# Optimization experiments

Hardware: AMD Instinct MI355X
Metric: run time of the kernel (lower is better)

The kernel has to match this reference:

```python
import jax, jax.numpy as jnp
import numpy as np

N_SRC, N_TGT, N_EDGES = 100000, 50000, 600000
IN_CH, OUT_CH = 128, 128
NUM_EDGE_TYPES, NUM_NODE_TYPES = 7, 4


def setup_inputs() -> dict:
    key = jax.random.key(0)
    ks = jax.random.split(key, 9)
    x_src = jax.random.normal(ks[0], (N_SRC, IN_CH), dtype=jnp.float32)
    x_target = jax.random.normal(ks[1], (N_TGT, IN_CH), dtype=jnp.float32)
    # PyG Linear: y = x @ W.T (+ b); W has shape (out, in)
    rel_w = jax.random.normal(ks[2], (NUM_EDGE_TYPES, OUT_CH, IN_CH), dtype=jnp.float32) * 0.05
    root_w = jax.random.normal(ks[3], (NUM_NODE_TYPES, OUT_CH, IN_CH), dtype=jnp.float32) * 0.05
    root_b = jax.random.normal(ks[4], (NUM_NODE_TYPES, OUT_CH), dtype=jnp.float32) * 0.05
    edge_src = jax.random.randint(ks[5], (N_EDGES,), 0, N_SRC, dtype=jnp.int32)
    edge_dst = jax.random.randint(ks[6], (N_EDGES,), 0, N_TGT, dtype=jnp.int32)
    edge_type = jax.random.randint(ks[7], (N_EDGES,), 0, NUM_EDGE_TYPES, dtype=jnp.int32)
    target_node_type = jax.random.randint(ks[8], (N_TGT,), 0, NUM_NODE_TYPES, dtype=jnp.int32)
    return {
        "x_src": x_src, "x_target": x_target,
        "rel_w": rel_w, "root_w": root_w, "root_b": root_b,
        "edge_src": edge_src, "edge_dst": edge_dst,
        "edge_type": edge_type, "target_node_type": target_node_type,
    }


def reference(x_src, x_target, rel_w, root_w, root_b,
              edge_src, edge_dst, edge_type, target_node_type):
    n_tgt = x_target.shape[0]
    num_rel = rel_w.shape[0]
    num_ntypes = root_w.shape[0]
    # Gather source features once for all edges: (E, in)
    msg = x_src[edge_src]
    out = jnp.zeros((n_tgt, rel_w.shape[1]), dtype=x_target.dtype)
    # Per-relation linear transform + scatter-MEAN over that relation's edges
    # (matches one propagate(aggr='mean') call per edge type: nodes with no
    #  incoming edges of type r contribute 0 for that relation).
    for r in range(num_rel):
        mask = (edge_type == r).astype(msg.dtype)  # (E,)
        y = (msg * mask[:, None]) @ rel_w[r].T     # (E, out)
        s = jax.ops.segment_sum(y, edge_dst, num_segments=n_tgt)
        cnt = jax.ops.segment_sum(mask, edge_dst, num_segments=n_tgt)
        out = out + s / jnp.maximum(cnt, 1.0)[:, None]
    # Per-node-type root linear (with bias), masked add
    for t in range(num_ntypes):
        m = (target_node_type == t)
        root = x_target @ root_w[t].T + root_b[t]
        out = out + jnp.where(m[:, None], root, 0.0)
    return out
```

## Files before the change

### kernel.cpp

```cpp
#include <hip/hip_runtime.h>

#define NSRC 100000
#define NTGT 50000
#define NE   600000
#define CH   128
#define NREL 7
#define NTYP 4
#define NP   (NREL * NTGT)
#define NB   ((NP + 1023) / 1024)
#define MAXBLK ((NTGT + 63) / 64)

typedef __attribute__((ext_vector_type(4))) float f32x4;
typedef __attribute__((ext_vector_type(8))) short bf16x8;
typedef unsigned int uint;
typedef unsigned short ushort;

static constexpr size_t A256(size_t x) { return (x + 255) & ~(size_t)255; }
static constexpr size_t CNT_O   = 0;
static constexpr size_t TCNT_O  = A256(CNT_O + (size_t)NP * 4);
static constexpr size_t ZERO_END= TCNT_O + 256;
static constexpr size_t BSE_O   = ZERO_END;
static constexpr size_t BSR_O   = A256(BSE_O + (size_t)NB * 4);
static constexpr size_t BBE_O   = A256(BSR_O + (size_t)NB * 4);
static constexpr size_t BBR_O   = A256(BBE_O + (size_t)NB * 4);
static constexpr size_t CUR_O   = A256(BBR_O + (size_t)NB * 4);
static constexpr size_t PLO_O   = A256(CUR_O + (size_t)NP * 4);
static constexpr size_t PN_O    = A256(PLO_O + (size_t)NP * 4);
static constexpr size_t PINV_O  = A256(PN_O + (size_t)NP * 4);
static constexpr size_t PDST_O  = A256(PINV_O + (size_t)NP * 4);
static constexpr size_t RELO_O  = A256(PDST_O + (size_t)NP * 4);
static constexpr size_t BKT_O   = A256(RELO_O + 64);
static constexpr size_t SEDGE_O = A256(BKT_O + (size_t)NTYP * NTGT * 4);
static constexpr size_t WB_O    = A256(SEDGE_O + (size_t)NE * 4);
static constexpr size_t XB_O    = A256(WB_O + (size_t)(NREL + NTYP) * CH * CH * 2);
static constexpr size_t XTB_O   = A256(XB_O + (size_t)NSRC * CH * 2);

__device__ __forceinline__ uint bfpack(float a, float b) {
  uint ua = __float_as_uint(a); ua = (ua + 0x7fff + ((ua >> 16) & 1)) >> 16;
  uint ub = __float_as_uint(b); ub = (ub + 0x7fff + ((ub >> 16) & 1)) >> 16;
  return ua | (ub << 16);
}
__device__ __forceinline__ ushort f2b(float x) {
  uint u = __float_as_uint(x);
  return (ushort)((u + 0x7fff + ((u >> 16) & 1)) >> 16);
}
__device__ __forceinline__ float bl(uint u) { return __uint_as_float(u << 16); }
__device__ __forceinline__ float bh(uint u) { return __uint_as_float(u & 0xffff0000u); }

__global__ void k_count(const int* __restrict__ edst, const int* __restrict__ etyp,
                        int* __restrict__ cnt) {
  int i = blockIdx.x * 256 + threadIdx.x;
  if (i < NE) atomicAdd(&cnt[etyp[i] * NTGT + edst[i]], 1);
}

__global__ void k_bucket(const int* __restrict__ ntyp, int* __restrict__ tcnt,
                         int* __restrict__ bucket) {
  __shared__ int lcnt[NTYP];
  __shared__ int lbase[NTYP];
  int v = blockIdx.x * 256 + threadIdx.x;
  if (threadIdx.x < NTYP) lcnt[threadIdx.x] = 0;
  __syncthreads();
  int t = 0, r = 0;
  bool ok = v < NTGT;
  if (ok) { t = ntyp[v]; r = atomicAdd(&lcnt[t], 1); }
  __syncthreads();
  if (threadIdx.x < NTYP) lbase[threadIdx.x] = atomicAdd(&tcnt[threadIdx.x], lcnt[threadIdx.x]);
  __syncthreads();
  if (ok) bucket[t * NTGT + lbase[t] + r] = v;
}

__global__ __launch_bounds__(256) void k_s1(const int* __restrict__ cnt,
                                            int* __restrict__ bsE, int* __restrict__ bsR) {
  __shared__ int sE[256], sR[256];
  int t = threadIdx.x, p0 = blockIdx.x * 1024 + t * 4;
  int e = 0, r = 0;
#pragma unroll
  for (int j = 0; j < 4; ++j) {
    int p = p0 + j;
    if (p < NP) { int c = cnt[p]; e += c; r += (c > 0); }
  }
  sE[t] = e; sR[t] = r; __syncthreads();
  for (int s = 128; s > 0; s >>= 1) {
    if (t < s) { sE[t] += sE[t + s]; sR[t] += sR[t + s]; }
    __syncthreads();
  }
  if (t == 0) { bsE[blockIdx.x] = sE[0]; bsR[blockIdx.x] = sR[0]; }
}

__global__ __launch_bounds__(512) void k_s2(const int* __restrict__ bsE, const int* __restrict__ bsR,
                                            int* __restrict__ bbE, int* __restrict__ bbR,
                                            int* __restrict__ reloff) {
  __shared__ int sE[512], sR[512];
  int t = threadIdx.x;
  int e = (t < NB) ? bsE[t] : 0;
  int r = (t < NB) ? bsR[t] : 0;
  sE[t] = e; sR[t] = r; __syncthreads();
  for (int s = 1; s < 512; s <<= 1) {
    int ae = 0, ar = 0;
    if (t >= s) { ae = sE[t - s]; ar = sR[t - s]; }
    __syncthreads();
    sE[t] += ae; sR[t] += ar;
    __syncthreads();
  }
  if (t < NB) { bbE[t] = sE[t] - e; bbR[t] = sR[t] - r; }
  if (t == NB - 1) reloff[NREL] = sR[t];
}

__global__ __launch_bounds__(256) void k_s3(const int* __restrict__ cnt,
    const int* __restrict__ bbE, const int* __restrict__ bbR,
    int* __restrict__ cur, int* __restrict__ plo, int* __restrict__ pn,
    float* __restrict__ pinv, int* __restrict__ pdst, int* __restrict__ reloff) {
  __shared__ int sE[256], sR[256];
  int t = threadIdx.x, p0 = blockIdx.x * 1024 + t * 4;
  int c[4]; int e = 0, r = 0;
#pragma unroll
  for (int j = 0; j < 4; ++j) {
    int p = p0 + j;
    c[j] = (p < NP) ? cnt[p] : 0;
    e += c[j]; r += (c[j] > 0);
  }
  sE[t] = e; sR[t] = r; __syncthreads();
  for (int s = 1; s < 256; s <<= 1) {
    int ae = 0, ar = 0;
    if (t >= s) { ae = sE[t - s]; ar = sR[t - s]; }
    __syncthreads();
    sE[t] += ae; sR[t] += ar;
    __syncthreads();
  }
  int baseE = bbE[blockIdx.x] + sE[t] - e;
  int baseR = bbR[blockIdx.x] + sR[t] - r;
#pragma unroll
  for (int j = 0; j < 4; ++j) {
    int p = p0 + j;
    if (p < NP) {
      cur[p] = baseE;
      if ((p % NTGT) == 0) reloff[p / NTGT] = baseR;
      if (c[j] > 0) {
        plo[baseR] = baseE; pn[baseR] = c[j];
        pinv[baseR] = 1.0f / (float)c[j];
        pdst[baseR] = p % NTGT;
        baseR++;
      }
      baseE += c[j];
    }
  }
}

__global__ void k_esort(const int* __restrict__ esrc, const int* __restrict__ edst,
                        const int* __restrict__ etyp, int* __restrict__ cur,
                        int* __restrict__ sedge) {
  int i = blockIdx.x * 256 + threadIdx.x;
  if (i < NE) {
    int p = etyp[i] * NTGT + edst[i];
    int pos = atomicAdd(&cur[p], 1);
    sedge[pos] = esrc[i];
  }
}

__global__ void k_conv(const float* __restrict__ xsrc, const float* __restrict__ xt,
                       const float* __restrict__ relw, const float* __restrict__ rootw,
                       ushort* __restrict__ xb, ushort* __restrict__ xtb,
                       ushort* __restrict__ wb) {
  const long long NXB = (long long)NSRC * CH / 4;
  const long long NXT = (long long)NTGT * CH / 4;
  const long long NWR = (long long)NREL * CH * CH / 4;
  const long long NWT = (long long)NTYP * CH * CH / 4;
  long long i4 = (long long)blockIdx.x * 256 + threadIdx.x;
  const float* src; ushort* dst; long long off;
  if (i4 < NXB) { src = xsrc; dst = xb; off = i4; }
  else if (i4 < NXB + NXT) { src = xt; dst = xtb; off = i4 - NXB; }
  else if (i4 < NXB + NXT + NWR) { src = relw; dst = wb; off = i4 - NXB - NXT; }
  else if (i4 < NXB + NXT + NWR + NWT) {
    src = rootw; dst = wb + (size_t)NREL * CH * CH; off = i4 - NXB - NXT - NWR;
  } else return;
  float4 v = *(const float4*)(src + off * 4);
  uint lo = (uint)f2b(v.x) | ((uint)f2b(v.y) << 16);
  uint hi = (uint)f2b(v.z) | ((uint)f2b(v.w) << 16);
  uint2 o = make_uint2(lo, hi);
  *(uint2*)(dst + off * 4) = o;
}

__global__ void k_init(const float* __restrict__ rootb, const int* __restrict__ ntyp,
                       float* __restrict__ out) {
  int idx = blockIdx.x * 256 + threadIdx.x;
  if (idx >= NTGT * 32) return;
  int v = idx >> 5, c4 = (idx & 31) << 2;
  int t = ntyp[v];
  *(float4*)(out + (size_t)v * CH + c4) = *(const float4*)(rootb + (size_t)t * CH + c4);
}

__device__ __forceinline__ void mfma_tail(const ushort* strip, const ushort* W,
                                          int m, int quad, const int* rowmap,
                                          float* __restrict__ out) {
  bf16x8 aF[4];
#pragma unroll
  for (int ks = 0; ks < 4; ++ks) {
    int c = ks * 4 + quad;
    aF[ks] = *(const bf16x8*)&strip[(m * 16 + (c ^ m)) << 3];
  }
  f32x4 acc[8];
#pragma unroll
  for (int ct = 0; ct < 8; ++ct) acc[ct] = (f32x4){0.f, 0.f, 0.f, 0.f};
#pragma unroll
  for (int ct = 0; ct < 8; ++ct) {
    int n = ct * 16 + m;
#pragma unroll
    for (int ks = 0; ks < 4; ++ks) {
      bf16x8 bF = *(const bf16x8*)(W + (size_t)n * CH + ks * 32 + quad * 8);
      acc[ct] = __builtin_amdgcn_mfma_f32_16x16x32_bf16(aF[ks], bF, acc[ct], 0, 0, 0);
    }
  }
#pragma unroll
  for (int ct = 0; ct < 8; ++ct)
#pragma unroll
    for (int reg = 0; reg < 4; ++reg)
      if (rowmap[reg] >= 0)
        unsafeAtomicAdd(&out[(size_t)rowmap[reg] * CH + ct * 16 + m], acc[ct][reg]);
}

__global__ __launch_bounds__(256) void k_mega(const ushort* __restrict__ xb,
    const ushort* __restrict__ xtb, const ushort* __restrict__ wb,
    const int* __restrict__ plo, const int* __restrict__ pn,
    const float* __restrict__ pinv, const int* __restrict__ pdst,
    const int* __restrict__ reloff, const int* __restrict__ sedge,
    const int* __restrict__ bucket, const int* __restrict__ tcnt,
    float* __restrict__ out) {
  __shared__ ushort As[4 * 16 * CH];
  int wv = threadIdx.x >> 6, ln = threadIdx.x & 63;
  ushort* strip = As + wv * (16 * CH);
  int m = ln & 15, quad = ln >> 4;
  int y = blockIdx.y;

  if (y < NREL) {
    int rel = y;
    int base = reloff[rel], relend = reloff[rel + 1];
    int row0 = blockIdx.x * 64;
    if (row0 >= relend - base) return;
    for (int i = 0; i < 16; ++i) {
      int gr = base + row0 + wv * 16 + i;
      float ax = 0.f, ay = 0.f, inv = 0.f;
      if (gr < relend) {
        int lo = plo[gr], n = pn[gr];
        inv = pinv[gr];
        const int* sp = sedge + lo;
        int q = 0;
        for (; q + 1 < n; q += 2) {
          int s0 = sp[q], s1 = sp[q + 1];
          uint u0 = *(const uint*)(xb + (size_t)s0 * CH + (ln << 1));
          uint u1 = *(const uint*)(xb + (size_t)s1 * CH + (ln << 1));
          ax += bl(u0) + bl(u1);
          ay += bh(u0) + bh(u1);
        }
        if (q < n) {
          uint u0 = *(const uint*)(xb + (size_t)sp[q] * CH + (ln << 1));
          ax += bl(u0); ay += bh(u0);
        }
      }
      uint w = bfpack(ax * inv, ay * inv);
      int c = ln >> 2;
      *(uint*)&strip[((i * 16 + (c ^ i)) << 3) + ((ln & 3) << 1)] = w;
    }
    int rowmap[4];
#pragma unroll
    for (int reg = 0; reg < 4; ++reg) {
      int gro = base + row0 + wv * 16 + quad * 4 + reg;
      rowmap[reg] = (gro < relend) ? pdst[gro] : -1;
    }
    mfma_tail(strip, wb + (size_t)rel * CH * CH, m, quad, rowmap, out);
  } else {
    int typ = y - NREL;
    int nb = tcnt[typ];
    int row0 = blockIdx.x * 64;
    if (row0 >= nb) return;
    const int* bk = bucket + (size_t)typ * NTGT;
    for (int i = 0; i < 16; ++i) {
      int rr = row0 + wv * 16 + i;
      uint w = 0;
      if (rr < nb) {
        int v = bk[rr];
        w = *(const uint*)(xtb + (size_t)v * CH + (ln << 1));
      }
      int c = ln >> 2;
      *(uint*)&strip[((i * 16 + (c ^ i)) << 3) + ((ln & 3) << 1)] = w;
    }
    int rowmap[4];
#pragma unroll
    for (int reg = 0; reg < 4; ++reg) {
      int rro = row0 + wv * 16 + quad * 4 + reg;
      rowmap[reg] = (rro < nb) ? bk[rro] : -1;
    }
    mfma_tail(strip, wb + (size_t)(NREL + typ) * CH * CH, m, quad, rowmap, out);
  }
}

extern "C" void kernel_launch(void* const* d_in, const int* in_sizes, int n_in,
                              void* d_out, int out_size, void* d_ws, size_t ws_size,
                              hipStream_t stream) {
  (void)in_sizes; (void)n_in; (void)out_size; (void)ws_size;
  const float* xsrc  = (const float*)d_in[0];
  const float* xt    = (const float*)d_in[1];
  const float* relw  = (const float*)d_in[2];
  const float* rootw = (const float*)d_in[3];
  const float* rootb = (const float*)d_in[4];
  const int* esrc = (const int*)d_in[5];
  const int* edst = (const int*)d_in[6];
  const int* etyp = (const int*)d_in[7];
  const int* ntyp = (const int*)d_in[8];
  float* out = (float*)d_out;

  char* ws = (char*)d_ws;
  int*   cnt    = (int*)(ws + CNT_O);
  int*   tcnt   = (int*)(ws + TCNT_O);
  int*   bsE    = (int*)(ws + BSE_O);
  int*   bsR    = (int*)(ws + BSR_O);
  int*   bbE    = (int*)(ws + BBE_O);
  int*   bbR    = (int*)(ws + BBR_O);
  int*   cur    = (int*)(ws + CUR_O);
  int*   plo    = (int*)(ws + PLO_O);
  int*   pn     = (int*)(ws + PN_O);
  float* pinv   = (float*)(ws + PINV_O);
  int*   pdst   = (int*)(ws + PDST_O);
  int*   reloff = (int*)(ws + RELO_O);
  int*   bucket = (int*)(ws + BKT_O);
  int*   sedge  = (int*)(ws + SEDGE_O);
  ushort* wb    = (ushort*)(ws + WB_O);
  ushort* xb    = (ushort*)(ws + XB_O);
  ushort* xtb   = (ushort*)(ws + XTB_O);

  hipMemsetAsync(ws, 0, ZERO_END, stream);
  k_count<<<dim3((NE + 255) / 256), dim3(256), 0, stream>>>(edst, etyp, cnt);
  k_bucket<<<dim3((NTGT + 255) / 256), dim3(256), 0, stream>>>(ntyp, tcnt, bucket);
  k_s1<<<dim3(NB), dim3(256), 0, stream>>>(cnt, bsE, bsR);
  k_s2<<<dim3(1), dim3(512), 0, stream>>>(bsE, bsR, bbE, bbR, reloff);
  k_s3<<<dim3(NB), dim3(256), 0, stream>>>(cnt, bbE, bbR, cur, plo, pn, pinv, pdst, reloff);
  k_esort<<<dim3((NE + 255) / 256), dim3(256), 0, stream>>>(esrc, edst, etyp, cur, sedge);
  {
    long long tot4 = (long long)NSRC * CH / 4 + (long long)NTGT * CH / 4 +
                     (long long)(NREL + NTYP) * CH * CH / 4;
    k_conv<<<dim3((unsigned)((tot4 + 255) / 256)), dim3(256), 0, stream>>>(
        xsrc, xt, relw, rootw, xb, xtb, wb);
  }
  k_init<<<dim3((NTGT * 32 + 255) / 256), dim3(256), 0, stream>>>(rootb, ntyp, out);
  k_mega<<<dim3(MAXBLK, NREL + NTYP), dim3(256), 0, stream>>>(
      xb, xtb, wb, plo, pn, pinv, pdst, reloff, sedge, bucket, tcnt, out);
}
```

Baseline: 411.9 us.

## Fuse per-relation and root transforms into destination-tiled kernel with register accumulation

Replaces the compacted per-(relation,destination) row scheme, the node-type buckets, out initialization and the global float atomics with one kernel per 32-destination tile. For each relation the kernel scatters gathered source rows into a shared-memory aggregate with LDS atomics, scales by the inverse count, and accumulates the MFMA result in registers. It then runs the four root-type transforms on the same tile, masked by node type, and writes output with the bias exactly once. This drops global atomics and several prep kernels. In exchange every tile runs all 7 relations and all 4 root types, including empty or masked ones, uses LDS atomics, and launches with only 128-thread blocks.

```diff
diff --git a/kernel.cpp b/kernel.cpp
--- a/kernel.cpp
+++ b/kernel.cpp
@@ -8,7 +8,8 @@
 #define NTYP 4
 #define NP   (NREL * NTGT)
 #define NB   ((NP + 1023) / 1024)
-#define MAXBLK ((NTGT + 63) / 64)
+#define TR   32
+#define NTILE ((NTGT + TR - 1) / TR)
 
 typedef __attribute__((ext_vector_type(4))) float f32x4;
 typedef __attribute__((ext_vector_type(8))) short bf16x8;
@@ -17,21 +18,13 @@
 
 static constexpr size_t A256(size_t x) { return (x + 255) & ~(size_t)255; }
 static constexpr size_t CNT_O   = 0;
-static constexpr size_t TCNT_O  = A256(CNT_O + (size_t)NP * 4);
-static constexpr size_t ZERO_END= TCNT_O + 256;
-static constexpr size_t BSE_O   = ZERO_END;
-static constexpr size_t BSR_O   = A256(BSE_O + (size_t)NB * 4);
-static constexpr size_t BBE_O   = A256(BSR_O + (size_t)NB * 4);
-static constexpr size_t BBR_O   = A256(BBE_O + (size_t)NB * 4);
-static constexpr size_t CUR_O   = A256(BBR_O + (size_t)NB * 4);
-static constexpr size_t PLO_O   = A256(CUR_O + (size_t)NP * 4);
-static constexpr size_t PN_O    = A256(PLO_O + (size_t)NP * 4);
-static constexpr size_t PINV_O  = A256(PN_O + (size_t)NP * 4);
-static constexpr size_t PDST_O  = A256(PINV_O + (size_t)NP * 4);
-static constexpr size_t RELO_O  = A256(PDST_O + (size_t)NP * 4);
-static constexpr size_t BKT_O   = A256(RELO_O + 64);
-static constexpr size_t SEDGE_O = A256(BKT_O + (size_t)NTYP * NTGT * 4);
-static constexpr size_t WB_O    = A256(SEDGE_O + (size_t)NE * 4);
+static constexpr size_t ZERO_END= A256(CNT_O + (size_t)NP * 4);
+static constexpr size_t EOFF_O  = ZERO_END;
+static constexpr size_t CUR_O   = A256(EOFF_O + (size_t)(NP + 64) * 4);
+static constexpr size_t BSE_O   = A256(CUR_O + (size_t)NP * 4);
+static constexpr size_t BBE_O   = A256(BSE_O + (size_t)NB * 4);
+static constexpr size_t SEDGE_O = A256(BBE_O + (size_t)NB * 4);
+static constexpr size_t WB_O    = A256(SEDGE_O + (size_t)NE * 8);
 static constexpr size_t XB_O    = A256(WB_O + (size_t)(NREL + NTYP) * CH * CH * 2);
 static constexpr size_t XTB_O   = A256(XB_O + (size_t)NSRC * CH * 2);
 
@@ -53,94 +46,66 @@
   if (i < NE) atomicAdd(&cnt[etyp[i] * NTGT + edst[i]], 1);
 }
 
-__global__ void k_bucket(const int* __restrict__ ntyp, int* __restrict__ tcnt,
-                         int* __restrict__ bucket) {
-  __shared__ int lcnt[NTYP];
-  __shared__ int lbase[NTYP];
-  int v = blockIdx.x * 256 + threadIdx.x;
-  if (threadIdx.x < NTYP) lcnt[threadIdx.x] = 0;
-  __syncthreads();
-  int t = 0, r = 0;
-  bool ok = v < NTGT;
-  if (ok) { t = ntyp[v]; r = atomicAdd(&lcnt[t], 1); }
-  __syncthreads();
-  if (threadIdx.x < NTYP) lbase[threadIdx.x] = atomicAdd(&tcnt[threadIdx.x], lcnt[threadIdx.x]);
-  __syncthreads();
-  if (ok) bucket[t * NTGT + lbase[t] + r] = v;
-}
-
 __global__ __launch_bounds__(256) void k_s1(const int* __restrict__ cnt,
-                                            int* __restrict__ bsE, int* __restrict__ bsR) {
-  __shared__ int sE[256], sR[256];
+                                            int* __restrict__ bsE) {
+  __shared__ int sE[256];
   int t = threadIdx.x, p0 = blockIdx.x * 1024 + t * 4;
-  int e = 0, r = 0;
+  int e = 0;
 #pragma unroll
   for (int j = 0; j < 4; ++j) {
     int p = p0 + j;
-    if (p < NP) { int c = cnt[p]; e += c; r += (c > 0); }
-  }
-  sE[t] = e; sR[t] = r; __syncthreads();
+    if (p < NP) e += cnt[p];
+  }
+  sE[t] = e; __syncthreads();
   for (int s = 128; s > 0; s >>= 1) {
-    if (t < s) { sE[t] += sE[t + s]; sR[t] += sR[t + s]; }
-    __syncthreads();
-  }
-  if (t == 0) { bsE[blockIdx.x] = sE[0]; bsR[blockIdx.x] = sR[0]; }
-}
-
-__global__ __launch_bounds__(512) void k_s2(const int* __restrict__ bsE, const int* __restrict__ bsR,
-                                            int* __restrict__ bbE, int* __restrict__ bbR,
-                                            int* __restrict__ reloff) {
-  __shared__ int sE[512], sR[512];
+    if (t < s) sE[t] += sE[t + s];
+    __syncthreads();
+  }
+  if (t == 0) bsE[blockIdx.x] = sE[0];
+}
+
+__global__ __launch_bounds__(512) void k_s2(const int* __restrict__ bsE,
+                                            int* __restrict__ bbE, int* __restrict__ eoff) {
+  __shared__ int sE[512];
   int t = threadIdx.x;
   int e = (t < NB) ? bsE[t] : 0;
-  int r = (t < NB) ? bsR[t] : 0;
-  sE[t] = e; sR[t] = r; __syncthreads();
+  sE[t] = e; __syncthreads();
   for (int s = 1; s < 512; s <<= 1) {
-    int ae = 0, ar = 0;
-    if (t >= s) { ae = sE[t - s]; ar = sR[t - s]; }
-    __syncthreads();
-    sE[t] += ae; sR[t] += ar;
-    __syncthreads();
-  }
-  if (t < NB) { bbE[t] = sE[t] - e; bbR[t] = sR[t] - r; }
-  if (t == NB - 1) reloff[NREL] = sR[t];
+    int ae = 0;
+    if (t >= s) ae = sE[t - s];
+    __syncthreads();
+    sE[t] += ae;
+    __syncthreads();
+  }
+  if (t < NB) bbE[t] = sE[t] - e;
+  if (t == 0) eoff[NP] = NE;
 }
 
 __global__ __launch_bounds__(256) void k_s3(const int* __restrict__ cnt,
-    const int* __restrict__ bbE, const int* __restrict__ bbR,
-    int* __restrict__ cur, int* __restrict__ plo, int* __restrict__ pn,
-    float* __restrict__ pinv, int* __restrict__ pdst, int* __restrict__ reloff) {
-  __shared__ int sE[256], sR[256];
+    const int* __restrict__ bbE, int* __restrict__ eoff, int* __restrict__ cur) {
+  __shared__ int sE[256];
   int t = threadIdx.x, p0 = blockIdx.x * 1024 + t * 4;
-  int c[4]; int e = 0, r = 0;
+  int c[4]; int e = 0;
 #pragma unroll
   for (int j = 0; j < 4; ++j) {
     int p = p0 + j;
     c[j] = (p < NP) ? cnt[p] : 0;
-    e += c[j]; r += (c[j] > 0);
-  }
-  sE[t] = e; sR[t] = r; __syncthreads();
+    e += c[j];
+  }
+  sE[t] = e; __syncthreads();
   for (int s = 1; s < 256; s <<= 1) {
-    int ae = 0, ar = 0;
-    if (t >= s) { ae = sE[t - s]; ar = sR[t - s]; }
-    __syncthreads();
-    sE[t] += ae; sR[t] += ar;
+    int ae = 0;
+    if (t >= s) ae = sE[t - s];
+    __syncthreads();
+    sE[t] += ae;
     __syncthreads();
   }
   int baseE = bbE[blockIdx.x] + sE[t] - e;
-  int baseR = bbR[blockIdx.x] + sR[t] - r;
 #pragma unroll
   for (int j = 0; j < 4; ++j) {
     int p = p0 + j;
     if (p < NP) {
-      cur[p] = baseE;
-      if ((p % NTGT) == 0) reloff[p / NTGT] = baseR;
-      if (c[j] > 0) {
-        plo[baseR] = baseE; pn[baseR] = c[j];
-        pinv[baseR] = 1.0f / (float)c[j];
-        pdst[baseR] = p % NTGT;
-        baseR++;
-      }
+      eoff[p] = baseE; cur[p] = baseE;
       baseE += c[j];
     }
   }
@@ -148,12 +113,13 @@
 
 __global__ void k_esort(const int* __restrict__ esrc, const int* __restrict__ edst,
                         const int* __restrict__ etyp, int* __restrict__ cur,
-                        int* __restrict__ sedge) {
+                        uint2* __restrict__ sedge) {
   int i = blockIdx.x * 256 + threadIdx.x;
   if (i < NE) {
-    int p = etyp[i] * NTGT + edst[i];
+    int d = edst[i];
+    int p = etyp[i] * NTGT + d;
     int pos = atomicAdd(&cur[p], 1);
-    sedge[pos] = esrc[i];
+    sedge[pos] = make_uint2((uint)esrc[i], (uint)d);
   }
 }
 
@@ -176,120 +142,130 @@
   float4 v = *(const float4*)(src + off * 4);
   uint lo = (uint)f2b(v.x) | ((uint)f2b(v.y) << 16);
   uint hi = (uint)f2b(v.z) | ((uint)f2b(v.w) << 16);
-  uint2 o = make_uint2(lo, hi);
-  *(uint2*)(dst + off * 4) = o;
-}
-
-__global__ void k_init(const float* __restrict__ rootb, const int* __restrict__ ntyp,
-                       float* __restrict__ out) {
-  int idx = blockIdx.x * 256 + threadIdx.x;
-  if (idx >= NTGT * 32) return;
-  int v = idx >> 5, c4 = (idx & 31) << 2;
-  int t = ntyp[v];
-  *(float4*)(out + (size_t)v * CH + c4) = *(const float4*)(rootb + (size_t)t * CH + c4);
-}
-
-__device__ __forceinline__ void mfma_tail(const ushort* strip, const ushort* W,
-                                          int m, int quad, const int* rowmap,
-                                          float* __restrict__ out) {
-  bf16x8 aF[4];
-#pragma unroll
-  for (int ks = 0; ks < 4; ++ks) {
-    int c = ks * 4 + quad;
-    aF[ks] = *(const bf16x8*)&strip[(m * 16 + (c ^ m)) << 3];
-  }
+  *(uint2*)(dst + off * 4) = make_uint2(lo, hi);
+}
+
+__global__ __launch_bounds__(128) void k_main(const ushort* __restrict__ xb,
+    const ushort* __restrict__ xtb, const ushort* __restrict__ wb,
+    const int* __restrict__ eoff, const uint2* __restrict__ sedge,
+    const int* __restrict__ ntyp, const float* __restrict__ rootb,
+    float* __restrict__ out) {
+  __shared__ float agg[TR * CH];
+  __shared__ ushort strip[2 * 16 * CH];
+  __shared__ float rb[NTYP * CH];
+  int wv = threadIdx.x >> 6, ln = threadIdx.x & 63;
+  int m = ln & 15, quad = ln >> 4;
+  int d0 = blockIdx.x * TR;
+  ushort* mystrip = strip + wv * 16 * CH;
+
+  ((f32x4*)rb)[threadIdx.x] = ((const f32x4*)rootb)[threadIdx.x];
+
   f32x4 acc[8];
 #pragma unroll
   for (int ct = 0; ct < 8; ++ct) acc[ct] = (f32x4){0.f, 0.f, 0.f, 0.f};
-#pragma unroll
-  for (int ct = 0; ct < 8; ++ct) {
-    int n = ct * 16 + m;
-#pragma unroll
-    for (int ks = 0; ks < 4; ++ks) {
-      bf16x8 bF = *(const bf16x8*)(W + (size_t)n * CH + ks * 32 + quad * 8);
-      acc[ct] = __builtin_amdgcn_mfma_f32_16x16x32_bf16(aF[ks], bF, acc[ct], 0, 0, 0);
-    }
-  }
-#pragma unroll
-  for (int ct = 0; ct < 8; ++ct)
-#pragma unroll
-    for (int reg = 0; reg < 4; ++reg)
-      if (rowmap[reg] >= 0)
-        unsafeAtomicAdd(&out[(size_t)rowmap[reg] * CH + ct * 16 + m], acc[ct][reg]);
-}
-
-__global__ __launch_bounds__(256) void k_mega(const ushort* __restrict__ xb,
-    const ushort* __restrict__ xtb, const ushort* __restrict__ wb,
-    const int* __restrict__ plo, const int* __restrict__ pn,
-    const float* __restrict__ pinv, const int* __restrict__ pdst,
-    const int* __restrict__ reloff, const int* __restrict__ sedge,
-    const int* __restrict__ bucket, const int* __restrict__ tcnt,
-    float* __restrict__ out) {
-  __shared__ ushort As[4 * 16 * CH];
-  int wv = threadIdx.x >> 6, ln = threadIdx.x & 63;
-  ushort* strip = As + wv * (16 * CH);
-  int m = ln & 15, quad = ln >> 4;
-  int y = blockIdx.y;
-
-  if (y < NREL) {
-    int rel = y;
-    int base = reloff[rel], relend = reloff[rel + 1];
-    int row0 = blockIdx.x * 64;
-    if (row0 >= relend - base) return;
-    for (int i = 0; i < 16; ++i) {
-      int gr = base + row0 + wv * 16 + i;
-      float ax = 0.f, ay = 0.f, inv = 0.f;
-      if (gr < relend) {
-        int lo = plo[gr], n = pn[gr];
-        inv = pinv[gr];
-        const int* sp = sedge + lo;
-        int q = 0;
-        for (; q + 1 < n; q += 2) {
-          int s0 = sp[q], s1 = sp[q + 1];
-          uint u0 = *(const uint*)(xb + (size_t)s0 * CH + (ln << 1));
-          uint u1 = *(const uint*)(xb + (size_t)s1 * CH + (ln << 1));
-          ax += bl(u0) + bl(u1);
-          ay += bh(u0) + bh(u1);
-        }
-        if (q < n) {
-          uint u0 = *(const uint*)(xb + (size_t)sp[q] * CH + (ln << 1));
-          ax += bl(u0); ay += bh(u0);
-        }
+
+  for (int r = 0; r < NREL; ++r) {
+#pragma unroll
+    for (int i = 0; i < TR * CH / (128 * 4); ++i)
+      *(f32x4*)&agg[(i * 128 + threadIdx.x) * 4] = (f32x4){0.f, 0.f, 0.f, 0.f};
+    __syncthreads();
+
+    int p0 = r * NTGT + d0;
+    int dhi = (d0 + TR < NTGT) ? d0 + TR : NTGT;
+    int lo = eoff[p0], hi = eoff[r * NTGT + dhi];
+    int n = hi - lo;
+    int half = (n + 1) >> 1;
+    int s0 = lo + wv * half;
+    int e1 = lo + ((wv == 0) ? half : n);
+    int i = s0;
+    for (; i + 1 < e1; i += 2) {
+      uint2 a = sedge[i], b = sedge[i + 1];
+      uint ua = *(const uint*)(xb + (size_t)a.x * CH + (ln << 1));
+      uint ub = *(const uint*)(xb + (size_t)b.x * CH + (ln << 1));
+      int ra = (int)a.y - d0, rbw = (int)b.y - d0;
+      atomicAdd(&agg[ra * CH + ln], bl(ua));
+      atomicAdd(&agg[ra * CH + 64 + ln], bh(ua));
+      atomicAdd(&agg[rbw * CH + ln], bl(ub));
+      atomicAdd(&agg[rbw * CH + 64 + ln], bh(ub));
+    }
+    if (i < e1) {
+      uint2 a = sedge[i];
+      uint ua = *(const uint*)(xb + (size_t)a.x * CH + (ln << 1));
+      int ra = (int)a.y - d0;
+      atomicAdd(&agg[ra * CH + ln], bl(ua));
+      atomicAdd(&agg[ra * CH + 64 + ln], bh(ua));
+    }
+    __syncthreads();
+
+    for (int ii = 0; ii < 16; ++ii) {
+      int d = d0 + wv * 16 + ii;
+      float inv = 0.f;
+      if (d < NTGT) {
+        int pp = r * NTGT + d;
+        int c = eoff[pp + 1] - eoff[pp];
+        inv = (c > 0) ? 1.0f / (float)c : 0.f;
       }
-      uint w = bfpack(ax * inv, ay * inv);
+      int row = wv * 16 + ii;
+      float ax = agg[row * CH + ln] * inv;
+      float ay = agg[row * CH + 64 + ln] * inv;
+      uint w = bfpack(ax, ay);
       int c = ln >> 2;
-      *(uint*)&strip[((i * 16 + (c ^ i)) << 3) + ((ln & 3) << 1)] = w;
-    }
-    int rowmap[4];
-#pragma unroll
-    for (int reg = 0; reg < 4; ++reg) {
-      int gro = base + row0 + wv * 16 + quad * 4 + reg;
-      rowmap[reg] = (gro < relend) ? pdst[gro] : -1;
-    }
-    mfma_tail(strip, wb + (size_t)rel * CH * CH, m, quad, rowmap, out);
-  } else {
-    int typ = y - NREL;
-    int nb = tcnt[typ];
-    int row0 = blockIdx.x * 64;
-    if (row0 >= nb) return;
-    const int* bk = bucket + (size_t)typ * NTGT;
-    for (int i = 0; i < 16; ++i) {
-      int rr = row0 + wv * 16 + i;
+      *(uint*)&mystrip[((ii * 16 + (c ^ ii)) << 3) + ((ln & 3) << 1)] = w;
+    }
+    __syncthreads();
+
+    bf16x8 aF[4];
+#pragma unroll
+    for (int ks = 0; ks < 4; ++ks)
+      aF[ks] = *(const bf16x8*)&mystrip[(m * 16 + ((ks * 4 + quad) ^ m)) << 3];
+    const ushort* W = wb + (size_t)r * CH * CH;
+#pragma unroll
+    for (int ct = 0; ct < 8; ++ct) {
+      int nn = ct * 16 + m;
+#pragma unroll
+      for (int ks = 0; ks < 4; ++ks) {
+        bf16x8 bF = *(const bf16x8*)(W + (size_t)nn * CH + ks * 32 + quad * 8);
+        acc[ct] = __builtin_amdgcn_mfma_f32_16x16x32_bf16(aF[ks], bF, acc[ct], 0, 0, 0);
+      }
+    }
+  }
+
+  for (int t = 0; t < NTYP; ++t) {
+    for (int ii = 0; ii < 16; ++ii) {
+      int d = d0 + wv * 16 + ii;
       uint w = 0;
-      if (rr < nb) {
-        int v = bk[rr];
-        w = *(const uint*)(xtb + (size_t)v * CH + (ln << 1));
+      if (d < NTGT && ntyp[d] == t)
+        w = *(const uint*)(xtb + (size_t)d * CH + (ln << 1));
+      int c = ln >> 2;
+      *(uint*)&mystrip[((ii * 16 + (c ^ ii)) << 3) + ((ln & 3) << 1)] = w;
+    }
+    bf16x8 aF[4];
+#pragma unroll
+    for (int ks = 0; ks < 4; ++ks)
+      aF[ks] = *(const bf16x8*)&mystrip[(m * 16 + ((ks * 4 + quad) ^ m)) << 3];
+    const ushort* W = wb + (size_t)(NREL + t) * CH * CH;
+#pragma unroll
+    for (int ct = 0; ct < 8; ++ct) {
+      int nn = ct * 16 + m;
+#pragma unroll
+      for (int ks = 0; ks < 4; ++ks) {
+        bf16x8 bF = *(const bf16x8*)(W + (size_t)nn * CH + ks * 32 + quad * 8);
+        acc[ct] = __builtin_amdgcn_mfma_f32_16x16x32_bf16(aF[ks], bF, acc[ct], 0, 0, 0);
       }
-      int c = ln >> 2;
-      *(uint*)&strip[((i * 16 + (c ^ i)) << 3) + ((ln & 3) << 1)] = w;
-    }
-    int rowmap[4];
-#pragma unroll
-    for (int reg = 0; reg < 4; ++reg) {
-      int rro = row0 + wv * 16 + quad * 4 + reg;
-      rowmap[reg] = (rro < nb) ? bk[rro] : -1;
-    }
-    mfma_tail(strip, wb + (size_t)(NREL + typ) * CH * CH, m, quad, rowmap, out);
+    }
+  }
+
+#pragma unroll
+  for (int reg = 0; reg < 4; ++reg) {
+    int d = d0 + wv * 16 + quad * 4 + reg;
+    if (d < NTGT) {
+      int t = ntyp[d];
+#pragma unroll
+      for (int ct = 0; ct < 8; ++ct) {
+        int col = ct * 16 + m;
+        out[(size_t)d * CH + col] = acc[ct][reg] + rb[t * CH + col];
+      }
+    }
   }
 }
 
@@ -309,30 +285,21 @@
   float* out = (float*)d_out;
 
   char* ws = (char*)d_ws;
-  int*   cnt    = (int*)(ws + CNT_O);
-  int*   tcnt   = (int*)(ws + TCNT_O);
-  int*   bsE    = (int*)(ws + BSE_O);
-  int*   bsR    = (int*)(ws + BSR_O);
-  int*   bbE    = (int*)(ws + BBE_O);
-  int*   bbR    = (int*)(ws + BBR_O);
-  int*   cur    = (int*)(ws + CUR_O);
-  int*   plo    = (int*)(ws + PLO_O);
-  int*   pn     = (int*)(ws + PN_O);
-  float* pinv   = (float*)(ws + PINV_O);
-  int*   pdst   = (int*)(ws + PDST_O);
-  int*   reloff = (int*)(ws + RELO_O);
-  int*   bucket = (int*)(ws + BKT_O);
-  int*   sedge  = (int*)(ws + SEDGE_O);
-  ushort* wb    = (ushort*)(ws + WB_O);
-  ushort* xb    = (ushort*)(ws + XB_O);
-  ushort* xtb   = (ushort*)(ws + XTB_O);
+  int*   cnt   = (int*)(ws + CNT_O);
+  int*   eoff  = (int*)(ws + EOFF_O);
+  int*   cur   = (int*)(ws + CUR_O);
+  int*   bsE   = (int*)(ws + BSE_O);
+  int*   bbE   = (int*)(ws + BBE_O);
+  uint2* sedge = (uint2*)(ws + SEDGE_O);
+  ushort* wb   = (ushort*)(ws + WB_O);
+  ushort* xb   = (ushort*)(ws + XB_O);
+  ushort* xtb  = (ushort*)(ws + XTB_O);
 
   hipMemsetAsync(ws, 0, ZERO_END, stream);
   k_count<<<dim3((NE + 255) / 256), dim3(256), 0, stream>>>(edst, etyp, cnt);
-  k_bucket<<<dim3((NTGT + 255) / 256), dim3(256), 0, stream>>>(ntyp, tcnt, bucket);
-  k_s1<<<dim3(NB), dim3(256), 0, stream>>>(cnt, bsE, bsR);
-  k_s2<<<dim3(1), dim3(512), 0, stream>>>(bsE, bsR, bbE, bbR, reloff);
-  k_s3<<<dim3(NB), dim3(256), 0, stream>>>(cnt, bbE, bbR, cur, plo, pn, pinv, pdst, reloff);
+  k_s1<<<dim3(NB), dim3(256), 0, stream>>>(cnt, bsE);
+  k_s2<<<dim3(1), dim3(512), 0, stream>>>(bsE, bbE, eoff);
+  k_s3<<<dim3(NB), dim3(256), 0, stream>>>(cnt, bbE, eoff, cur);
   k_esort<<<dim3((NE + 255) / 256), dim3(256), 0, stream>>>(esrc, edst, etyp, cur, sedge);
   {
     long long tot4 = (long long)NSRC * CH / 4 + (long long)NTGT * CH / 4 +
@@ -340,7 +307,5 @@
     k_conv<<<dim3((unsigned)((tot4 + 255) / 256)), dim3(256), 0, stream>>>(
         xsrc, xt, relw, rootw, xb, xtb, wb);
   }
-  k_init<<<dim3((NTGT * 32 + 255) / 256), dim3(256), 0, stream>>>(rootb, ntyp, out);
-  k_mega<<<dim3(MAXBLK, NREL + NTYP), dim3(256), 0, stream>>>(
-      xb, xtb, wb, plo, pn, pinv, pdst, reloff, sedge, bucket, tcnt, out);
-}
+  k_main<<<dim3(NTILE), dim3(128), 0, stream>>>(xb, xtb, wb, eoff, sedge, ntyp, rootb, out);
+}
```

Result: slower. 862.3 us (+109.3%).

## Aggregate edges via LDS atomics per tile and drop node-type bucketing

Applied to the files above, without the earlier changes.

The main kernel now gives each 64-row tile the contiguous span of sorted edges and has each wave stream edges into a shared-memory float accumulator with LDS atomics. This replaces the old scheme where each wave walked rows one at a time with a variable-length inner loop. The sorted edge records now carry their destination row id, so the per-row count array is no longer needed. Root-type handling no longer buckets nodes: each tile runs MFMA against all four root weight matrices with masked inputs, which quadruples that small GEMM work but removes a kernel. Bias init is folded into the conversion kernel, and the 32KB LDS tile plus LDS atomic contention may reduce occupancy.

```diff
diff --git a/kernel.cpp b/kernel.cpp
--- a/kernel.cpp
+++ b/kernel.cpp
@@ -8,7 +8,7 @@
 #define NTYP 4
 #define NP   (NREL * NTGT)
 #define NB   ((NP + 1023) / 1024)
-#define MAXBLK ((NTGT + 63) / 64)
+#define NTILE ((NTGT + 63) / 64)
 
 typedef __attribute__((ext_vector_type(4))) float f32x4;
 typedef __attribute__((ext_vector_type(8))) short bf16x8;
@@ -17,21 +17,19 @@
 
 static constexpr size_t A256(size_t x) { return (x + 255) & ~(size_t)255; }
 static constexpr size_t CNT_O   = 0;
-static constexpr size_t TCNT_O  = A256(CNT_O + (size_t)NP * 4);
-static constexpr size_t ZERO_END= TCNT_O + 256;
+static constexpr size_t ZERO_END= A256(CNT_O + (size_t)NP * 4);
 static constexpr size_t BSE_O   = ZERO_END;
 static constexpr size_t BSR_O   = A256(BSE_O + (size_t)NB * 4);
 static constexpr size_t BBE_O   = A256(BSR_O + (size_t)NB * 4);
 static constexpr size_t BBR_O   = A256(BBE_O + (size_t)NB * 4);
 static constexpr size_t CUR_O   = A256(BBR_O + (size_t)NB * 4);
 static constexpr size_t PLO_O   = A256(CUR_O + (size_t)NP * 4);
-static constexpr size_t PN_O    = A256(PLO_O + (size_t)NP * 4);
-static constexpr size_t PINV_O  = A256(PN_O + (size_t)NP * 4);
+static constexpr size_t PINV_O  = A256(PLO_O + (size_t)NP * 4);
 static constexpr size_t PDST_O  = A256(PINV_O + (size_t)NP * 4);
-static constexpr size_t RELO_O  = A256(PDST_O + (size_t)NP * 4);
-static constexpr size_t BKT_O   = A256(RELO_O + 64);
-static constexpr size_t SEDGE_O = A256(BKT_O + (size_t)NTYP * NTGT * 4);
-static constexpr size_t WB_O    = A256(SEDGE_O + (size_t)NE * 4);
+static constexpr size_t RID_O   = A256(PDST_O + (size_t)NP * 4);
+static constexpr size_t RELO_O  = A256(RID_O + (size_t)NP * 4);
+static constexpr size_t SEDGE_O = A256(RELO_O + 64);
+static constexpr size_t WB_O    = A256(SEDGE_O + (size_t)NE * 8);
 static constexpr size_t XB_O    = A256(WB_O + (size_t)(NREL + NTYP) * CH * CH * 2);
 static constexpr size_t XTB_O   = A256(XB_O + (size_t)NSRC * CH * 2);
 
@@ -51,22 +49,6 @@
                         int* __restrict__ cnt) {
   int i = blockIdx.x * 256 + threadIdx.x;
   if (i < NE) atomicAdd(&cnt[etyp[i] * NTGT + edst[i]], 1);
-}
-
-__global__ void k_bucket(const int* __restrict__ ntyp, int* __restrict__ tcnt,
-                         int* __restrict__ bucket) {
-  __shared__ int lcnt[NTYP];
-  __shared__ int lbase[NTYP];
-  int v = blockIdx.x * 256 + threadIdx.x;
-  if (threadIdx.x < NTYP) lcnt[threadIdx.x] = 0;
-  __syncthreads();
-  int t = 0, r = 0;
-  bool ok = v < NTGT;
-  if (ok) { t = ntyp[v]; r = atomicAdd(&lcnt[t], 1); }
-  __syncthreads();
-  if (threadIdx.x < NTYP) lbase[threadIdx.x] = atomicAdd(&tcnt[threadIdx.x], lcnt[threadIdx.x]);
-  __syncthreads();
-  if (ok) bucket[t * NTGT + lbase[t] + r] = v;
 }
 
 __global__ __launch_bounds__(256) void k_s1(const int* __restrict__ cnt,
@@ -108,8 +90,8 @@
 
 __global__ __launch_bounds__(256) void k_s3(const int* __restrict__ cnt,
     const int* __restrict__ bbE, const int* __restrict__ bbR,
-    int* __restrict__ cur, int* __restrict__ plo, int* __restrict__ pn,
-    float* __restrict__ pinv, int* __restrict__ pdst, int* __restrict__ reloff) {
+    int* __restrict__ cur, int* __restrict__ plo, float* __restrict__ pinv,
+    int* __restrict__ pdst, int* __restrict__ rowid, int* __restrict__ reloff) {
   __shared__ int sE[256], sR[256];
   int t = threadIdx.x, p0 = blockIdx.x * 1024 + t * 4;
   int c[4]; int e = 0, r = 0;
@@ -136,9 +118,10 @@
       cur[p] = baseE;
       if ((p % NTGT) == 0) reloff[p / NTGT] = baseR;
       if (c[j] > 0) {
-        plo[baseR] = baseE; pn[baseR] = c[j];
+        plo[baseR] = baseE;
         pinv[baseR] = 1.0f / (float)c[j];
         pdst[baseR] = p % NTGT;
+        rowid[p] = baseR;
         baseR++;
       }
       baseE += c[j];
@@ -147,24 +130,26 @@
 }
 
 __global__ void k_esort(const int* __restrict__ esrc, const int* __restrict__ edst,
-                        const int* __restrict__ etyp, int* __restrict__ cur,
-                        int* __restrict__ sedge) {
+                        const int* __restrict__ etyp, const int* __restrict__ rowid,
+                        int* __restrict__ cur, uint2* __restrict__ sedge) {
   int i = blockIdx.x * 256 + threadIdx.x;
   if (i < NE) {
     int p = etyp[i] * NTGT + edst[i];
     int pos = atomicAdd(&cur[p], 1);
-    sedge[pos] = esrc[i];
-  }
-}
-
-__global__ void k_conv(const float* __restrict__ xsrc, const float* __restrict__ xt,
+    sedge[pos] = make_uint2((uint)esrc[i], (uint)rowid[p]);
+  }
+}
+
+__global__ void k_prep(const float* __restrict__ xsrc, const float* __restrict__ xt,
                        const float* __restrict__ relw, const float* __restrict__ rootw,
+                       const float* __restrict__ rootb, const int* __restrict__ ntyp,
                        ushort* __restrict__ xb, ushort* __restrict__ xtb,
-                       ushort* __restrict__ wb) {
+                       ushort* __restrict__ wb, float* __restrict__ out) {
   const long long NXB = (long long)NSRC * CH / 4;
   const long long NXT = (long long)NTGT * CH / 4;
   const long long NWR = (long long)NREL * CH * CH / 4;
   const long long NWT = (long long)NTYP * CH * CH / 4;
+  const long long NBI = (long long)NTGT * CH / 4;
   long long i4 = (long long)blockIdx.x * 256 + threadIdx.x;
   const float* src; ushort* dst; long long off;
   if (i4 < NXB) { src = xsrc; dst = xb; off = i4; }
@@ -172,124 +157,144 @@
   else if (i4 < NXB + NXT + NWR) { src = relw; dst = wb; off = i4 - NXB - NXT; }
   else if (i4 < NXB + NXT + NWR + NWT) {
     src = rootw; dst = wb + (size_t)NREL * CH * CH; off = i4 - NXB - NXT - NWR;
+  } else if (i4 < NXB + NXT + NWR + NWT + NBI) {
+    long long o = (i4 - NXB - NXT - NWR - NWT) * 4;
+    int d = (int)(o >> 7), c = (int)(o & 127);
+    int t = ntyp[d];
+    *(float4*)(out + (size_t)d * CH + c) = *(const float4*)(rootb + (size_t)t * CH + c);
+    return;
   } else return;
   float4 v = *(const float4*)(src + off * 4);
   uint lo = (uint)f2b(v.x) | ((uint)f2b(v.y) << 16);
   uint hi = (uint)f2b(v.z) | ((uint)f2b(v.w) << 16);
-  uint2 o = make_uint2(lo, hi);
-  *(uint2*)(dst + off * 4) = o;
-}
-
-__global__ void k_init(const float* __restrict__ rootb, const int* __restrict__ ntyp,
-                       float* __restrict__ out) {
-  int idx = blockIdx.x * 256 + threadIdx.x;
-  if (idx >= NTGT * 32) return;
-  int v = idx >> 5, c4 = (idx & 31) << 2;
-  int t = ntyp[v];
-  *(float4*)(out + (size_t)v * CH + c4) = *(const float4*)(rootb + (size_t)t * CH + c4);
-}
-
-__device__ __forceinline__ void mfma_tail(const ushort* strip, const ushort* W,
-                                          int m, int quad, const int* rowmap,
-                                          float* __restrict__ out) {
-  bf16x8 aF[4];
-#pragma unroll
-  for (int ks = 0; ks < 4; ++ks) {
-    int c = ks * 4 + quad;
-    aF[ks] = *(const bf16x8*)&strip[(m * 16 + (c ^ m)) << 3];
-  }
+  *(uint2*)(dst + off * 4) = make_uint2(lo, hi);
+}
+
+__global__ __launch_bounds__(256) void k_fuse(const ushort* __restrict__ xb,
+    const ushort* __restrict__ xtb, const ushort* __restrict__ wb,
+    const int* __restrict__ plo, const float* __restrict__ pinv,
+    const int* __restrict__ pdst, const int* __restrict__ reloff,
+    const uint2* __restrict__ sedge, const int* __restrict__ ntyp,
+    float* __restrict__ out) {
+  __shared__ float agg[64 * CH];
+  int u = blockIdx.x, ty = blockIdx.y;
+  int wv = threadIdx.x >> 6, ln = threadIdx.x & 63;
+  int m = ln & 15, quad = ln >> 4;
   f32x4 acc[8];
 #pragma unroll
   for (int ct = 0; ct < 8; ++ct) acc[ct] = (f32x4){0.f, 0.f, 0.f, 0.f};
-#pragma unroll
-  for (int ct = 0; ct < 8; ++ct) {
-    int n = ct * 16 + m;
+
+  if (u < NREL) {
+    int base = reloff[u], relend = reloff[u + 1];
+    int gr0 = base + ty * 64;
+    if (gr0 >= relend) return;
+    int total = reloff[NREL];
+    int grL = (gr0 + 63 < relend - 1) ? gr0 + 63 : relend - 1;
+
+#pragma unroll
+    for (int i = 0; i < 8; ++i)
+      ((f32x4*)agg)[i * 256 + threadIdx.x] = (f32x4){0.f, 0.f, 0.f, 0.f};
+    __syncthreads();
+
+    int elo = plo[gr0];
+    int ehi = (grL + 1 < total) ? plo[grL + 1] : NE;
+    int cj = ln >> 2, wi = ln & 3;
+    int i = elo + wv;
+    for (; i + 4 < ehi; i += 8) {
+      uint2 e0 = sedge[i], e1 = sedge[i + 4];
+      uint x0 = *(const uint*)(xb + (size_t)e0.x * CH + (ln << 1));
+      uint x1 = *(const uint*)(xb + (size_t)e1.x * CH + (ln << 1));
+      int r0 = (int)e0.y - gr0, r1 = (int)e1.y - gr0;
+      int a0 = r0 * CH + ((cj ^ (r0 & 15)) << 2) + wi;
+      int a1 = r1 * CH + ((cj ^ (r1 & 15)) << 2) + wi;
+      atomicAdd(&agg[a0], bl(x0));
+      atomicAdd(&agg[a0 + 64], bh(x0));
+      atomicAdd(&agg[a1], bl(x1));
+      atomicAdd(&agg[a1 + 64], bh(x1));
+    }
+    if (i < ehi) {
+      uint2 e0 = sedge[i];
+      uint x0 = *(const uint*)(xb + (size_t)e0.x * CH + (ln << 1));
+      int r0 = (int)e0.y - gr0;
+      int a0 = r0 * CH + ((cj ^ (r0 & 15)) << 2) + wi;
+      atomicAdd(&agg[a0], bl(x0));
+      atomicAdd(&agg[a0 + 64], bh(x0));
+    }
+    __syncthreads();
+
+    int row = wv * 16 + m;
+    int gr = gr0 + row;
+    float inv = (gr < relend) ? pinv[gr] : 0.f;
+    bf16x8 aF[4];
 #pragma unroll
     for (int ks = 0; ks < 4; ++ks) {
-      bf16x8 bF = *(const bf16x8*)(W + (size_t)n * CH + ks * 32 + quad * 8);
-      acc[ct] = __builtin_amdgcn_mfma_f32_16x16x32_bf16(aF[ks], bF, acc[ct], 0, 0, 0);
-    }
-  }
-#pragma unroll
-  for (int ct = 0; ct < 8; ++ct)
-#pragma unroll
-    for (int reg = 0; reg < 4; ++reg)
-      if (rowmap[reg] >= 0)
-        unsafeAtomicAdd(&out[(size_t)rowmap[reg] * CH + ct * 16 + m], acc[ct][reg]);
-}
-
-__global__ __launch_bounds__(256) void k_mega(const ushort* __restrict__ xb,
-    const ushort* __restrict__ xtb, const ushort* __restrict__ wb,
-    const int* __restrict__ plo, const int* __restrict__ pn,
-    const float* __restrict__ pinv, const int* __restrict__ pdst,
-    const int* __restrict__ reloff, const int* __restrict__ sedge,
-    const int* __restrict__ bucket, const int* __restrict__ tcnt,
-    float* __restrict__ out) {
-  __shared__ ushort As[4 * 16 * CH];
-  int wv = threadIdx.x >> 6, ln = threadIdx.x & 63;
-  ushort* strip = As + wv * (16 * CH);
-  int m = ln & 15, quad = ln >> 4;
-  int y = blockIdx.y;
-
-  if (y < NREL) {
-    int rel = y;
-    int base = reloff[rel], relend = reloff[rel + 1];
-    int row0 = blockIdx.x * 64;
-    if (row0 >= relend - base) return;
-    for (int i = 0; i < 16; ++i) {
-      int gr = base + row0 + wv * 16 + i;
-      float ax = 0.f, ay = 0.f, inv = 0.f;
-      if (gr < relend) {
-        int lo = plo[gr], n = pn[gr];
-        inv = pinv[gr];
-        const int* sp = sedge + lo;
-        int q = 0;
-        for (; q + 1 < n; q += 2) {
-          int s0 = sp[q], s1 = sp[q + 1];
-          uint u0 = *(const uint*)(xb + (size_t)s0 * CH + (ln << 1));
-          uint u1 = *(const uint*)(xb + (size_t)s1 * CH + (ln << 1));
-          ax += bl(u0) + bl(u1);
-          ay += bh(u0) + bh(u1);
-        }
-        if (q < n) {
-          uint u0 = *(const uint*)(xb + (size_t)sp[q] * CH + (ln << 1));
-          ax += bl(u0); ay += bh(u0);
+      int t = ks * 4 + quad;
+      f32x4 ev = *(const f32x4*)&agg[row * CH + ((t ^ m) << 2)];
+      f32x4 od = *(const f32x4*)&agg[row * CH + 64 + ((t ^ m) << 2)];
+      uint4 pk;
+      pk.x = bfpack(ev.x * inv, od.x * inv);
+      pk.y = bfpack(ev.y * inv, od.y * inv);
+      pk.z = bfpack(ev.z * inv, od.z * inv);
+      pk.w = bfpack(ev.w * inv, od.w * inv);
+      aF[ks] = *(bf16x8*)&pk;
+    }
+    const ushort* W = wb + (size_t)u * CH * CH;
+#pragma unroll
+    for (int ct = 0; ct < 8; ++ct) {
+      int nn = ct * 16 + m;
+#pragma unroll
+      for (int ks = 0; ks < 4; ++ks) {
+        bf16x8 bF = *(const bf16x8*)(W + (size_t)nn * CH + ks * 32 + quad * 8);
+        acc[ct] = __builtin_amdgcn_mfma_f32_16x16x32_bf16(aF[ks], bF, acc[ct], 0, 0, 0);
+      }
+    }
+    int dmap[4];
+#pragma unroll
+    for (int reg = 0; reg < 4; ++reg) {
+      int gre = gr0 + wv * 16 + quad * 4 + reg;
+      dmap[reg] = (gre < relend) ? pdst[gre] : -1;
+    }
+#pragma unroll
+    for (int ct = 0; ct < 8; ++ct)
+#pragma unroll
+      for (int reg = 0; reg < 4; ++reg)
+        if (dmap[reg] >= 0)
+          unsafeAtomicAdd(&out[(size_t)dmap[reg] * CH + ct * 16 + m], acc[ct][reg]);
+  } else {
+    int d0 = ty * 64;
+    int drow = d0 + wv * 16 + m;
+    bool okr = drow < NTGT;
+    int tmy = okr ? ntyp[drow] : -1;
+    bf16x8 zf;
+    *(uint4*)&zf = make_uint4(0, 0, 0, 0);
+    bf16x8 aF[4];
+#pragma unroll
+    for (int ks = 0; ks < 4; ++ks)
+      aF[ks] = okr ? *(const bf16x8*)(xtb + (size_t)drow * CH + (ks * 4 + quad) * 8) : zf;
+#pragma unroll
+    for (int t = 0; t < NTYP; ++t) {
+      bf16x8 aT[4];
+#pragma unroll
+      for (int ks = 0; ks < 4; ++ks) aT[ks] = (tmy == t) ? aF[ks] : zf;
+      const ushort* W = wb + (size_t)(NREL + t) * CH * CH;
+#pragma unroll
+      for (int ct = 0; ct < 8; ++ct) {
+        int nn = ct * 16 + m;
+#pragma unroll
+        for (int ks = 0; ks < 4; ++ks) {
+          bf16x8 bF = *(const bf16x8*)(W + (size_t)nn * CH + ks * 32 + quad * 8);
+          acc[ct] = __builtin_amdgcn_mfma_f32_16x16x32_bf16(aT[ks], bF, acc[ct], 0, 0, 0);
         }
       }
-      uint w = bfpack(ax * inv, ay * inv);
-      int c = ln >> 2;
-      *(uint*)&strip[((i * 16 + (c ^ i)) << 3) + ((ln & 3) << 1)] = w;
-    }
-    int rowmap[4];
+    }
 #pragma unroll
     for (int reg = 0; reg < 4; ++reg) {
-      int gro = base + row0 + wv * 16 + quad * 4 + reg;
-      rowmap[reg] = (gro < relend) ? pdst[gro] : -1;
-    }
-    mfma_tail(strip, wb + (size_t)rel * CH * CH, m, quad, rowmap, out);
-  } else {
-    int typ = y - NREL;
-    int nb = tcnt[typ];
-    int row0 = blockIdx.x * 64;
-    if (row0 >= nb) return;
-    const int* bk = bucket + (size_t)typ * NTGT;
-    for (int i = 0; i < 16; ++i) {
-      int rr = row0 + wv * 16 + i;
-      uint w = 0;
-      if (rr < nb) {
-        int v = bk[rr];
-        w = *(const uint*)(xtb + (size_t)v * CH + (ln << 1));
-      }
-      int c = ln >> 2;
-      *(uint*)&strip[((i * 16 + (c ^ i)) << 3) + ((ln & 3) << 1)] = w;
-    }
-    int rowmap[4];
-#pragma unroll
-    for (int reg = 0; reg < 4; ++reg) {
-      int rro = row0 + wv * 16 + quad * 4 + reg;
-      rowmap[reg] = (rro < nb) ? bk[rro] : -1;
-    }
-    mfma_tail(strip, wb + (size_t)(NREL + typ) * CH * CH, m, quad, rowmap, out);
+      int d = d0 + wv * 16 + quad * 4 + reg;
+      if (d < NTGT)
+#pragma unroll
+        for (int ct = 0; ct < 8; ++ct)
+          unsafeAtomicAdd(&out[(size_t)d * CH + ct * 16 + m], acc[ct][reg]);
+    }
   }
 }
 
@@ -310,37 +315,33 @@
 
   char* ws = (char*)d_ws;
   int*   cnt    = (int*)(ws + CNT_O);
-  int*   tcnt   = (int*)(ws + TCNT_O);
   int*   bsE    = (int*)(ws + BSE_O);
   int*   bsR    = (int*)(ws + BSR_O);
   int*   bbE    = (int*)(ws + BBE_O);
   int*   bbR    = (int*)(ws + BBR_O);
   int*   cur    = (int*)(ws + CUR_O);
   int*   plo    = (int*)(ws + PLO_O);
-  int*   pn     = (int*)(ws + PN_O);
   float* pinv   = (float*)(ws + PINV_O);
   int*   pdst   = (int*)(ws + PDST_O);
+  int*   rowid  = (int*)(ws + RID_O);
   int*   reloff = (int*)(ws + RELO_O);
-  int*   bucket = (int*)(ws + BKT_O);
-  int*   sedge  = (int*)(ws + SEDGE_O);
+  uint2* sedge  = (uint2*)(ws + SEDGE_O);
   ushort* wb    = (ushort*)(ws + WB_O);
   ushort* xb    = (ushort*)(ws + XB_O);
   ushort* xtb   = (ushort*)(ws + XTB_O);
 
   hipMemsetAsync(ws, 0, ZERO_END, stream);
   k_count<<<dim3((NE + 255) / 256), dim3(256), 0, stream>>>(edst, etyp, cnt);
-  k_bucket<<<dim3((NTGT + 255) / 256), dim3(256), 0, stream>>>(ntyp, tcnt, bucket);
   k_s1<<<dim3(NB), dim3(256), 0, stream>>>(cnt, bsE, bsR);
   k_s2<<<dim3(1), dim3(512), 0, stream>>>(bsE, bsR, bbE, bbR, reloff);
-  k_s3<<<dim3(NB), dim3(256), 0, stream>>>(cnt, bbE, bbR, cur, plo, pn, pinv, pdst, reloff);
-  k_esort<<<dim3((NE + 255) / 256), dim3(256), 0, stream>>>(esrc, edst, etyp, cur, sedge);
+  k_s3<<<dim3(NB), dim3(256), 0, stream>>>(cnt, bbE, bbR, cur, plo, pinv, pdst, rowid, reloff);
+  k_esort<<<dim3((NE + 255) / 256), dim3(256), 0, stream>>>(esrc, edst, etyp, rowid, cur, sedge);
   {
     long long tot4 = (long long)NSRC * CH / 4 + (long long)NTGT * CH / 4 +
-                     (long long)(NREL + NTYP) * CH * CH / 4;
-    k_conv<<<dim3((unsigned)((tot4 + 255) / 256)), dim3(256), 0, stream>>>(
-        xsrc, xt, relw, rootw, xb, xtb, wb);
-  }
-  k_init<<<dim3((NTGT * 32 + 255) / 256), dim3(256), 0, stream>>>(rootb, ntyp, out);
-  k_mega<<<dim3(MAXBLK, NREL + NTYP), dim3(256), 0, stream>>>(
-      xb, xtb, wb, plo, pn, pinv, pdst, reloff, sedge, bucket, tcnt, out);
-}
+                     (long long)(NREL + NTYP) * CH * CH / 4 + (long long)NTGT * CH / 4;
+    k_prep<<<dim3((unsigned)((tot4 + 255) / 256)), dim3(256), 0, stream>>>(
+        xsrc, xt, relw, rootw, rootb, ntyp, xb, xtb, wb, out);
+  }
+  k_fuse<<<dim3(NREL + 1, NTILE), dim3(256), 0, stream>>>(
+      xb, xtb, wb, plo, pinv, pdst, reloff, sedge, ntyp, out);
+}
```

Result: slower. 663.7 us (+61.1%).
